# Performance work log

Hardware: AMD Instinct MI355X
Metric: run time of the kernel (lower is better)

Reference implementation:

```python
import jax, jax.numpy as jnp
import numpy as np

B, S, D = 4, 1024, 768
H = 12
K = 64            # max relative distance
R = 2 * K + 1     # number of relative buckets
DH = D // H       # per-head dim (k_dim and v_dim both == d_model here)


def setup_inputs() -> dict:
    key = jax.random.key(0)
    ks = jax.random.split(key, 14)
    s = 0.02
    return {
        "query": jax.random.normal(ks[0], (B, S, D), jnp.float32),
        "key":   jax.random.normal(ks[1], (B, S, D), jnp.float32),
        "value": jax.random.normal(ks[2], (B, S, D), jnp.float32),
        "WQ_w": jax.random.normal(ks[3], (D, D), jnp.float32) * s,
        "WQ_b": jnp.zeros((D,), jnp.float32),
        "WK_w": jax.random.normal(ks[4], (D, D), jnp.float32) * s,
        "WK_b": jnp.zeros((D,), jnp.float32),
        "WV_w": jax.random.normal(ks[5], (D, D), jnp.float32) * s,
        "WV_b": jnp.zeros((D,), jnp.float32),
        "WO_w": jax.random.normal(ks[6], (D, D), jnp.float32) * s,
        "WO_b": jnp.zeros((D,), jnp.float32),
        "embK": jax.random.normal(ks[7], (R, D), jnp.float32) * s,
        "embV": jax.random.normal(ks[8], (R, D), jnp.float32) * s,
    }


def _split_heads(x):  # [B,S,D] -> [B,H,S,DH]
    b, s, _ = x.shape
    return x.reshape(b, s, H, DH).transpose(0, 2, 1, 3)


def reference(query, key, value, WQ_w, WQ_b, WK_w, WK_b, WV_w, WV_b, WO_w, WO_b, embK, embV):
    Q = _split_heads(query @ WQ_w.T + WQ_b)   # [B,H,Sq,DH]
    Kt = _split_heads(key @ WK_w.T + WK_b)    # [B,H,Sk,DH]
    V = _split_heads(value @ WV_w.T + WV_b)   # [B,H,Sk,DH]

    Sq, Sk = Q.shape[2], Kt.shape[2]
    # clipped relative position bucket index, matching get_relative_matrix
    idx = jnp.clip(jnp.arange(Sk)[None, :] - jnp.arange(Sq)[:, None], -K, K) + K  # [Sq,Sk]
    qrows = jnp.arange(Sq)[:, None]

    # content scores
    qk = jnp.einsum('bhqd,bhkd->bhqk', Q, Kt)
    # relative-K scores: project Q onto all R buckets, then gather per (q,k).
    # Mathematically identical to einsum('bhqd,hqkd->bhqk', Q, gather(embK)).
    embK_h = embK.reshape(R, H, DH)
    rel_all = jnp.einsum('bhqd,rhd->bhqr', Q, embK_h)        # [B,H,Sq,R]
    rel_scores = rel_all[:, :, qrows, idx]                   # [B,H,Sq,Sk]

    scores = (qk + rel_scores) / jnp.sqrt(jnp.asarray(DH, jnp.float32))
    attn = jax.nn.softmax(scores, axis=-1)                   # [B,H,Sq,Sk]

    out = jnp.einsum('bhqk,bhkv->bhqv', attn, V)             # [B,H,Sq,DH]
    # relative-V: scatter attention mass into R buckets per query, then one GEMM.
    w = jnp.zeros((B, H, Sq, R), attn.dtype).at[:, :, qrows, idx].add(attn)
    embV_h = embV.reshape(R, H, DH)
    out = out + jnp.einsum('bhqr,rhv->bhqv', w, embV_h)

    out = out.transpose(0, 2, 1, 3).reshape(B, Sq, D)        # merge heads
    out = out @ WO_w.T + WO_b                                 # (dropout p=0 is identity)
    return out, attn
```

## Files before the change

### kernel.cpp

```cpp
#include <hip/hip_runtime.h>

typedef _Float16 f16;
typedef _Float16 f16x4 __attribute__((ext_vector_type(4)));
typedef _Float16 f16x8 __attribute__((ext_vector_type(8)));
typedef float    f32x4 __attribute__((ext_vector_type(4)));

#define DEV static __device__ __forceinline__

DEV f32x4 mfma16(f16x8 a, f16x8 b, f32x4 c) {
    return __builtin_amdgcn_mfma_f32_16x16x32_f16(a, b, c, 0, 0, 0);
}

DEV void gload16(const f16* g, f16* l) {
    __builtin_amdgcn_global_load_lds(
        (const __attribute__((address_space(1))) unsigned int*)g,
        (__attribute__((address_space(3))) unsigned int*)l,
        16, 0, 0);
}


struct ConvArgs {
    const float* src[8];
    f16*         dst[8];
};

__global__ __launch_bounds__(256) void k_convert(ConvArgs a) {
    const int seg[9] = {0, 786432, 1572864, 2359296, 2506752, 2654208,
                        2801664, 2949120, 2973888};
    for (int i = blockIdx.x * 256 + threadIdx.x; i < 2973888; i += gridDim.x * 256) {
        int s = 0;
        while (i >= seg[s + 1]) s++;
        const int j = i - seg[s];
        const float4 v = ((const float4*)a.src[s])[j];
        f16x4 o;
        o[0] = (f16)v.x; o[1] = (f16)v.y; o[2] = (f16)v.z; o[3] = (f16)v.w;
        ((f16x4*)a.dst[s])[j] = o;
    }
}

__global__ __launch_bounds__(256) void k_embvt(const float* __restrict__ embV,
                                               f16* __restrict__ dst) {
    const int idx = blockIdx.x * 256 + threadIdx.x;
    if (idx >= 12 * 64 * 160) return;
    const int r  = idx % 160;
    const int dh = (idx / 160) % 64;
    const int h  = idx / (160 * 64);
    float v = 0.f;
    if (r < 129) v = embV[r * 768 + h * 64 + dh];
    dst[idx] = (f16)v;
}

#define GEMM_TILE_BODY(X, W)                                                   \
    const int tid = threadIdx.x;                                               \
    const int w = tid >> 6, l = tid & 63, quad = l >> 4, l16 = l & 15;         \
    const int wr = w >> 1, wc = w & 1;                                         \
    const int rl = l >> 2, cc = l & 3;                                         \
    const int csrc = (cc ^ ((rl ^ (rl >> 2)) & 3)) * 8;                        \
    const f16* gA = (X) + (size_t)(m0 + w * 32 + rl) * 768 + csrc;             \
    const f16* gB = (W) + (size_t)(n0 + w * 32 + rl) * 768 + csrc;             \
    f16* lA0 = As + (w * 32) * 32;                                             \
    f16* lA1 = As + (w * 32 + 16) * 32;                                        \
    f16* lB0 = Bs + (w * 32) * 32;                                             \
    f16* lB1 = Bs + (w * 32 + 16) * 32;                                        \
    const int xsw = (quad ^ ((l16 ^ (l16 >> 2)) & 3)) * 8;                     \
    f32x4 acc[4][4] = {};                                                      \
    for (int k0 = 0; k0 < 768; k0 += 32) {                                     \
        __syncthreads();                                                       \
        gload16(gA + k0, lA0);                                                 \
        gload16(gA + k0 + 16 * 768, lA1);                                      \
        gload16(gB + k0, lB0);                                                 \
        gload16(gB + k0 + 16 * 768, lB1);                                      \
        __syncthreads();                                                       \
        f16x8 af[4], bf[4];                                                    \
        _Pragma("unroll") for (int i = 0; i < 4; i++)                          \
            af[i] = *(const f16x8*)(As + (wr * 64 + i * 16 + l16) * 32 + xsw); \
        _Pragma("unroll") for (int i = 0; i < 4; i++)                          \
            bf[i] = *(const f16x8*)(Bs + (wc * 64 + i * 16 + l16) * 32 + xsw); \
        _Pragma("unroll") for (int i = 0; i < 4; i++)                          \
            _Pragma("unroll") for (int j = 0; j < 4; j++)                      \
                acc[i][j] = mfma16(af[i], bf[j], acc[i][j]);                   \
    }

__global__ __launch_bounds__(256) void k_gemm_qkv(
    const f16* __restrict__ xq, const f16* __restrict__ xk, const f16* __restrict__ xv,
    const f16* __restrict__ wq, const f16* __restrict__ wk, const f16* __restrict__ wv,
    const float* __restrict__ bq, const float* __restrict__ bk, const float* __restrict__ bv,
    f16* __restrict__ Qh, f16* __restrict__ Kh, f16* __restrict__ Vt) {
    __shared__ __align__(16) f16 As[128 * 32];
    __shared__ __align__(16) f16 Bs[128 * 32];

    const int t  = blockIdx.y / 6;
    const int n0 = (blockIdx.y % 6) * 128;
    const int m0 = blockIdx.x * 128;
    const f16*   X    = (t == 0) ? xq : (t == 1) ? xk : xv;
    const f16*   W    = (t == 0) ? wq : (t == 1) ? wk : wv;
    const float* bias = (t == 0) ? bq : (t == 1) ? bk : bv;

    GEMM_TILE_BODY(X, W)

#pragma unroll
    for (int j = 0; j < 4; j++) {
        const int   nj = n0 + wc * 64 + j * 16 + l16;
        const float bb = bias[nj];
        const int   h = nj >> 6, dh = nj & 63;
#pragma unroll
        for (int i = 0; i < 4; i++) {
            const int mb = m0 + wr * 64 + i * 16 + quad * 4;
            const int b = mb >> 10, s = mb & 1023;
            if (t < 2) {
                f16* dst = (t == 0) ? Qh : Kh;
                const int base = ((b * 12 + h) * 1024 + s) * 64 + dh;
#pragma unroll
                for (int r = 0; r < 4; r++)
                    dst[base + r * 64] = (f16)(acc[i][j][r] + bb);
            } else {
                f16x4 pk;
#pragma unroll
                for (int r = 0; r < 4; r++) pk[r] = (f16)(acc[i][j][r] + bb);
                *(f16x4*)(Vt + ((b * 12 + h) * 64 + dh) * 1024 + s) = pk;
            }
        }
    }
}

__global__ __launch_bounds__(256) void k_gemm_out(
    const f16* __restrict__ Xin, const f16* __restrict__ Win,
    const float* __restrict__ bias, float* __restrict__ out) {
    __shared__ __align__(16) f16 As[128 * 32];
    __shared__ __align__(16) f16 Bs[128 * 32];

    const int n0 = blockIdx.y * 128;
    const int m0 = blockIdx.x * 128;

    GEMM_TILE_BODY(Xin, Win)

#pragma unroll
    for (int j = 0; j < 4; j++) {
        const int   nj = n0 + wc * 64 + j * 16 + l16;
        const float bb = bias[nj];
#pragma unroll
        for (int i = 0; i < 4; i++) {
            const int mb = m0 + wr * 64 + i * 16 + quad * 4;
#pragma unroll
            for (int r = 0; r < 4; r++)
                out[(size_t)(mb + r) * 768 + nj] = acc[i][j][r] + bb;
        }
    }
}

constexpr int SCP = 1032;

__global__ __launch_bounds__(256) void k_attn(
    const f16* __restrict__ Qh, const f16* __restrict__ Kh, const f16* __restrict__ Vt,
    const f16* __restrict__ embK, const f16* __restrict__ embVt,
    float* __restrict__ attn, f16* __restrict__ ctx) {
    __shared__ __align__(16) f16 sc[16 * SCP];
    __shared__ __align__(16) f16 relw[16 * 160];
    __shared__ float red[3][4][16];
    __shared__ float invs[16], tl0[16], tl1[16];

    const int qt = blockIdx.x, bh = blockIdx.y;
    const int b = bh / 12, h = bh % 12;
    const int q0 = qt * 16;
    const int tid = threadIdx.x;
    const int w = tid >> 6, l = tid & 63, quad = l >> 4, l16 = l & 15;

    const f16* Qb = Qh + (bh * 1024 + q0) * 64;
    const f16* Kb = Kh + bh * 1024 * 64;
    const f16* Vb = Vt + bh * 64 * 1024;

    const f16x8 qa0 = *(const f16x8*)(Qb + l16 * 64 + quad * 8);
    const f16x8 qa1 = *(const f16x8*)(Qb + l16 * 64 + 32 + quad * 8);

    for (int nf = w; nf < 9; nf += 4) {
        const int r0 = nf * 16;
        int rr = r0 + l16; if (rr > 128) rr = 128;
        const f16x8 eb0 = *(const f16x8*)(embK + rr * 768 + h * 64 + quad * 8);
        const f16x8 eb1 = *(const f16x8*)(embK + rr * 768 + h * 64 + 32 + quad * 8);
        f32x4 a = {};
        a = mfma16(eb0, qa0, a);
        a = mfma16(eb1, qa1, a);
        f16x4 pk;
#pragma unroll
        for (int r = 0; r < 4; r++) pk[r] = (f16)a[r];
        *(f16x4*)(relw + l16 * 160 + r0 + quad * 4) = pk;
    }
    __syncthreads();

    const int qg = q0 + l16;
    const float cLog = 0.18033688f;
    const float rLo = (float)relw[l16 * 160]       * cLog;
    const float rHi = (float)relw[l16 * 160 + 128] * cLog;
    float rs = 0.f, rt0 = 0.f, rt1 = 0.f;
    const int dbase = w * 256 + quad * 4 - qg;
    for (int nf = 0; nf < 16; nf++) {
        const int kc = w * 256 + nf * 16;
        const f16x8 kf0 = *(const f16x8*)(Kb + (kc + l16) * 64 + quad * 8);
        const f16x8 kf1 = *(const f16x8*)(Kb + (kc + l16) * 64 + 32 + quad * 8);
        f32x4 a = {};
        a = mfma16(kf0, qa0, a);
        a = mfma16(kf1, qa1, a);
        const int d0 = dbase + nf * 16;
        float es[4];
        if (d0 >= 64) {
#pragma unroll
            for (int r = 0; r < 4; r++)
                es[r] = __builtin_amdgcn_exp2f(fmaf(a[r], cLog, rHi));
            const float s4 = (es[0] + es[1]) + (es[2] + es[3]);
            rs += s4; rt1 += s4;
        } else if (d0 <= -67) {
#pragma unroll
            for (int r = 0; r < 4; r++)
                es[r] = __builtin_amdgcn_exp2f(fmaf(a[r], cLog, rLo));
            const float s4 = (es[0] + es[1]) + (es[2] + es[3]);
            rs += s4; rt0 += s4;
        } else {
#pragma unroll
            for (int r = 0; r < 4; r++) {
                const int dr = d0 + r;
                const int drc = (dr < -64) ? -64 : (dr > 64) ? 64 : dr;
                const float rv = (float)relw[l16 * 160 + drc + 64] * cLog;
                const float e = __builtin_amdgcn_exp2f(fmaf(a[r], cLog, rv));
                es[r] = e;
                rs += e;
                rt0 += (dr <= -64) ? e : 0.f;
                rt1 += (dr >= 64) ? e : 0.f;
            }
        }
        f16x4 pk;
#pragma unroll
        for (int r = 0; r < 4; r++) pk[r] = (f16)es[r];
        *(f16x4*)(sc + l16 * SCP + kc + quad * 4) = pk;
    }
    rs  += __shfl_xor(rs, 16);  rs  += __shfl_xor(rs, 32);
    rt0 += __shfl_xor(rt0, 16); rt0 += __shfl_xor(rt0, 32);
    rt1 += __shfl_xor(rt1, 16); rt1 += __shfl_xor(rt1, 32);
    if (l < 16) {
        red[0][w][l16] = rs;
        red[1][w][l16] = rt0;
        red[2][w][l16] = rt1;
    }
    __syncthreads();
    if (tid < 16) {
        const float s = red[0][0][tid] + red[0][1][tid] + red[0][2][tid] + red[0][3][tid];
        invs[tid] = 1.f / s;
        tl0[tid] = red[1][0][tid] + red[1][1][tid] + red[1][2][tid] + red[1][3][tid];
        tl1[tid] = red[2][0][tid] + red[2][1][tid] + red[2][2][tid] + red[2][3][tid];
    }
    __syncthreads();

    {
        float* ab = attn + ((long)bh * 1024 + q0) * 1024;
#pragma unroll
        for (int rr = 0; rr < 4; rr++) {
            const int row = w * 4 + rr;
            const float inv = invs[row];
            const f16* p = sc + row * SCP;
            float* o = ab + (long)row * 1024;
#pragma unroll
            for (int jj = 0; jj < 4; jj++) {
                const int c = jj * 256 + l * 4;
                const f16x4 v = *(const f16x4*)(p + c);
                *(float4*)(o + c) = make_float4((float)v[0] * inv, (float)v[1] * inv,
                                                (float)v[2] * inv, (float)v[3] * inv);
            }
        }
    }
    for (int idx = tid; idx < 16 * 160; idx += 256) {
        const int row = idx / 160, r = idx - row * 160;
        float v = 0.f;
        if (r == 0) v = tl0[row];
        else if (r == 128) v = tl1[row];
        else if (r < 128) {
            const int col = q0 + row + r - 64;
            if (col >= 0 && col < 1024) v = (float)sc[row * SCP + col];
        }
        relw[idx] = (f16)v;
    }
    __syncthreads();

    {
        f32x4 a = {};
        const f16* vrow = Vb + (w * 16 + l16) * 1024;
        for (int ks = 0; ks < 32; ks++) {
            const f16x8 af = *(const f16x8*)(sc + l16 * SCP + ks * 32 + quad * 8);
            const f16x8 bf = *(const f16x8*)(vrow + ks * 32 + quad * 8);
            a = mfma16(af, bf, a);
        }
        const f16* erow = embVt + (h * 64 + w * 16 + l16) * 160;
#pragma unroll
        for (int ks = 0; ks < 5; ks++) {
            const f16x8 af = *(const f16x8*)(relw + l16 * 160 + ks * 32 + quad * 8);
            const f16x8 bf = *(const f16x8*)(erow + ks * 32 + quad * 8);
            a = mfma16(af, bf, a);
        }
#pragma unroll
        for (int r = 0; r < 4; r++) {
            const int row = quad * 4 + r;
            const int qg2 = q0 + row;
            ctx[(b * 1024 + qg2) * 768 + h * 64 + w * 16 + l16] = (f16)(a[r] * invs[row]);
        }
    }
}

extern "C" void kernel_launch(void* const* d_in, const int* in_sizes, int n_in,
                              void* d_out, int out_size, void* d_ws, size_t ws_size,
                              hipStream_t stream) {
    const float* q_in = (const float*)d_in[0];
    const float* k_in = (const float*)d_in[1];
    const float* v_in = (const float*)d_in[2];
    const float* WQw  = (const float*)d_in[3];
    const float* WQb  = (const float*)d_in[4];
    const float* WKw  = (const float*)d_in[5];
    const float* WKb  = (const float*)d_in[6];
    const float* WVw  = (const float*)d_in[7];
    const float* WVb  = (const float*)d_in[8];
    const float* WOw  = (const float*)d_in[9];
    const float* WOb  = (const float*)d_in[10];
    const float* embK = (const float*)d_in[11];
    const float* embV = (const float*)d_in[12];

    char*  ws  = (char*)d_ws;
    size_t off = 0;
    auto nxt = [&](size_t n) {
        char* p = ws + off;
        off += (n + 255) & ~(size_t)255;
        return p;
    };
    f16* qb    = (f16*)nxt(3145728 * 2);
    f16* kb    = (f16*)nxt(3145728 * 2);
    f16* vb    = (f16*)nxt(3145728 * 2);
    f16* Wqb   = (f16*)nxt(589824 * 2);
    f16* Wkb   = (f16*)nxt(589824 * 2);
    f16* Wvb   = (f16*)nxt(589824 * 2);
    f16* Wob   = (f16*)nxt(589824 * 2);
    f16* embKb = (f16*)nxt(99072 * 2);
    f16* embVt = (f16*)nxt(122880 * 2);
    f16* Qh    = (f16*)nxt(3145728 * 2);
    f16* Kh    = (f16*)nxt(3145728 * 2);
    f16* Vt    = (f16*)nxt(3145728 * 2);
    f16* ctx   = (f16*)nxt(3145728 * 2);
    (void)ws_size; (void)in_sizes; (void)n_in; (void)out_size;

    ConvArgs ca;
    ca.src[0] = q_in; ca.src[1] = k_in; ca.src[2] = v_in;
    ca.src[3] = WQw;  ca.src[4] = WKw;  ca.src[5] = WVw;
    ca.src[6] = WOw;  ca.src[7] = embK;
    ca.dst[0] = qb;   ca.dst[1] = kb;   ca.dst[2] = vb;
    ca.dst[3] = Wqb;  ca.dst[4] = Wkb;  ca.dst[5] = Wvb;
    ca.dst[6] = Wob;  ca.dst[7] = embKb;

    k_convert<<<dim3(2048), dim3(256), 0, stream>>>(ca);
    k_embvt<<<dim3(480), dim3(256), 0, stream>>>(embV, embVt);
    k_gemm_qkv<<<dim3(32, 18), dim3(256), 0, stream>>>(
        qb, kb, vb, Wqb, Wkb, Wvb, WQb, WKb, WVb, Qh, Kh, Vt);
    float* attn = (float*)d_out + 3145728;
    k_attn<<<dim3(64, 48), dim3(256), 0, stream>>>(Qh, Kh, Vt, embKb, embVt, attn, ctx);
    k_gemm_out<<<dim3(32, 6), dim3(256), 0, stream>>>(ctx, Wob, WOb, (float*)d_out);
}
```

Baseline: 396.7 us.

## Double-buffer GEMM LDS tiles and fuse embV transpose into convert kernel

The shared GEMM tile body now uses two LDS buffers, so the global-to-LDS loads for the next K slice are issued before the MFMA work on the current slice. Explicit vmcnt/lgkmcnt waits and barriers order the stages, replacing the two full syncthreads per iteration. Separately, the embV transpose/pad kernel is merged into the convert kernel as extra blocks, saving one launch. LDS use per block doubles, which may lower occupancy, and the hand-written waitcnt scheme depends on the exact number of outstanding loads.

Result: no change. 400.5 us (+1.0%).

```diff
diff --git a/kernel.cpp b/kernel.cpp
--- a/kernel.cpp
+++ b/kernel.cpp
@@ -24,10 +24,24 @@
     f16*         dst[8];
 };
 
-__global__ __launch_bounds__(256) void k_convert(ConvArgs a) {
+__global__ __launch_bounds__(256) void k_convert(ConvArgs a,
+                                                 const float* __restrict__ embV,
+                                                 f16* __restrict__ embVtd) {
+    const int bx = blockIdx.x;
+    if (bx >= 2048) {
+        const int idx = (bx - 2048) * 256 + threadIdx.x;
+        if (idx >= 12 * 64 * 160) return;
+        const int r  = idx % 160;
+        const int dh = (idx / 160) % 64;
+        const int h  = idx / (160 * 64);
+        float v = 0.f;
+        if (r < 129) v = embV[r * 768 + h * 64 + dh];
+        embVtd[idx] = (f16)v;
+        return;
+    }
     const int seg[9] = {0, 786432, 1572864, 2359296, 2506752, 2654208,
                         2801664, 2949120, 2973888};
-    for (int i = blockIdx.x * 256 + threadIdx.x; i < 2973888; i += gridDim.x * 256) {
+    for (int i = bx * 256 + threadIdx.x; i < 2973888; i += 2048 * 256) {
         int s = 0;
         while (i >= seg[s + 1]) s++;
         const int j = i - seg[s];
@@ -36,18 +50,6 @@
         o[0] = (f16)v.x; o[1] = (f16)v.y; o[2] = (f16)v.z; o[3] = (f16)v.w;
         ((f16x4*)a.dst[s])[j] = o;
     }
-}
-
-__global__ __launch_bounds__(256) void k_embvt(const float* __restrict__ embV,
-                                               f16* __restrict__ dst) {
-    const int idx = blockIdx.x * 256 + threadIdx.x;
-    if (idx >= 12 * 64 * 160) return;
-    const int r  = idx % 160;
-    const int dh = (idx / 160) % 64;
-    const int h  = idx / (160 * 64);
-    float v = 0.f;
-    if (r < 129) v = embV[r * 768 + h * 64 + dh];
-    dst[idx] = (f16)v;
 }
 
 #define GEMM_TILE_BODY(X, W)                                                   \
@@ -58,36 +60,48 @@
     const int csrc = (cc ^ ((rl ^ (rl >> 2)) & 3)) * 8;                        \
     const f16* gA = (X) + (size_t)(m0 + w * 32 + rl) * 768 + csrc;             \
     const f16* gB = (W) + (size_t)(n0 + w * 32 + rl) * 768 + csrc;             \
-    f16* lA0 = As + (w * 32) * 32;                                             \
-    f16* lA1 = As + (w * 32 + 16) * 32;                                        \
-    f16* lB0 = Bs + (w * 32) * 32;                                             \
-    f16* lB1 = Bs + (w * 32 + 16) * 32;                                        \
     const int xsw = (quad ^ ((l16 ^ (l16 >> 2)) & 3)) * 8;                     \
     f32x4 acc[4][4] = {};                                                      \
-    for (int k0 = 0; k0 < 768; k0 += 32) {                                     \
-        __syncthreads();                                                       \
-        gload16(gA + k0, lA0);                                                 \
-        gload16(gA + k0 + 16 * 768, lA1);                                      \
-        gload16(gB + k0, lB0);                                                 \
-        gload16(gB + k0 + 16 * 768, lB1);                                      \
-        __syncthreads();                                                       \
+    auto STAGE = [&](int pp, int kk) {                                         \
+        f16* lA = As + pp * 4096 + (w * 32) * 32;                              \
+        f16* lB = Bs + pp * 4096 + (w * 32) * 32;                              \
+        gload16(gA + kk, lA);                                                  \
+        gload16(gA + kk + 16 * 768, lA + 16 * 32);                             \
+        gload16(gB + kk, lB);                                                  \
+        gload16(gB + kk + 16 * 768, lB + 16 * 32);                             \
+    };                                                                         \
+    auto COMPUTE = [&](int pp) {                                               \
+        const f16* Ab = As + pp * 4096;                                        \
+        const f16* Bb = Bs + pp * 4096;                                        \
         f16x8 af[4], bf[4];                                                    \
         _Pragma("unroll") for (int i = 0; i < 4; i++)                          \
-            af[i] = *(const f16x8*)(As + (wr * 64 + i * 16 + l16) * 32 + xsw); \
+            af[i] = *(const f16x8*)(Ab + (wr * 64 + i * 16 + l16) * 32 + xsw); \
         _Pragma("unroll") for (int i = 0; i < 4; i++)                          \
-            bf[i] = *(const f16x8*)(Bs + (wc * 64 + i * 16 + l16) * 32 + xsw); \
+            bf[i] = *(const f16x8*)(Bb + (wc * 64 + i * 16 + l16) * 32 + xsw); \
         _Pragma("unroll") for (int i = 0; i < 4; i++)                          \
             _Pragma("unroll") for (int j = 0; j < 4; j++)                      \
                 acc[i][j] = mfma16(af[i], bf[j], acc[i][j]);                   \
-    }
+    };                                                                         \
+    STAGE(0, 0);                                                               \
+    _Pragma("unroll 1") for (int t = 0; t < 23; ++t) {                         \
+        STAGE((t + 1) & 1, (t + 1) * 32);                                      \
+        asm volatile("s_waitcnt vmcnt(4)" ::: "memory");                       \
+        __builtin_amdgcn_s_barrier();                                          \
+        COMPUTE(t & 1);                                                        \
+        asm volatile("s_waitcnt lgkmcnt(0)" ::: "memory");                     \
+        __builtin_amdgcn_s_barrier();                                          \
+    }                                                                          \
+    asm volatile("s_waitcnt vmcnt(0)" ::: "memory");                           \
+    __builtin_amdgcn_s_barrier();                                              \
+    COMPUTE(1);
 
 __global__ __launch_bounds__(256) void k_gemm_qkv(
     const f16* __restrict__ xq, const f16* __restrict__ xk, const f16* __restrict__ xv,
     const f16* __restrict__ wq, const f16* __restrict__ wk, const f16* __restrict__ wv,
     const float* __restrict__ bq, const float* __restrict__ bk, const float* __restrict__ bv,
     f16* __restrict__ Qh, f16* __restrict__ Kh, f16* __restrict__ Vt) {
-    __shared__ __align__(16) f16 As[128 * 32];
-    __shared__ __align__(16) f16 Bs[128 * 32];
+    __shared__ __align__(16) f16 As[2 * 128 * 32];
+    __shared__ __align__(16) f16 Bs[2 * 128 * 32];
 
     const int t  = blockIdx.y / 6;
     const int n0 = (blockIdx.y % 6) * 128;
@@ -126,8 +140,8 @@
 __global__ __launch_bounds__(256) void k_gemm_out(
     const f16* __restrict__ Xin, const f16* __restrict__ Win,
     const float* __restrict__ bias, float* __restrict__ out) {
-    __shared__ __align__(16) f16 As[128 * 32];
-    __shared__ __align__(16) f16 Bs[128 * 32];
+    __shared__ __align__(16) f16 As[2 * 128 * 32];
+    __shared__ __align__(16) f16 Bs[2 * 128 * 32];
 
     const int n0 = blockIdx.y * 128;
     const int m0 = blockIdx.x * 128;
@@ -350,8 +364,7 @@
     ca.dst[3] = Wqb;  ca.dst[4] = Wkb;  ca.dst[5] = Wvb;
     ca.dst[6] = Wob;  ca.dst[7] = embKb;
 
-    k_convert<<<dim3(2048), dim3(256), 0, stream>>>(ca);
-    k_embvt<<<dim3(480), dim3(256), 0, stream>>>(embV, embVt);
+    k_convert<<<dim3(2048 + 480), dim3(256), 0, stream>>>(ca, embV, embVt);
     k_gemm_qkv<<<dim3(32, 18), dim3(256), 0, stream>>>(
         qb, kb, vb, Wqb, Wkb, Wvb, WQb, WKb, WVb, Qh, Kh, Vt);
     float* attn = (float*)d_out + 3145728;
```
